# Kernel optimization log

Hardware: AMD Instinct MI355X
Metric: run time of the kernel (lower is better)

Reference implementation:

```python
import jax, jax.numpy as jnp
import numpy as np

D_MODEL = 512
NUM_HEADS = 8


def setup_inputs() -> dict:
    key = jax.random.key(0)
    ks = jax.random.split(key, 12)
    B, S, D = 2, 4096, D_MODEL
    scale = 1.0 / np.sqrt(D)
    inp = {
        "q": jax.random.normal(ks[0], (B, S, D), jnp.float32),
        "k": jax.random.normal(ks[1], (B, S, D), jnp.float32),
        "v": jax.random.normal(ks[2], (B, S, D), jnp.float32),
        "w_q": jax.random.normal(ks[3], (D, D), jnp.float32) * scale,
        "b_q": jax.random.normal(ks[4], (D,), jnp.float32) * scale,
        "w_k": jax.random.normal(ks[5], (D, D), jnp.float32) * scale,
        "b_k": jax.random.normal(ks[6], (D,), jnp.float32) * scale,
        "w_v": jax.random.normal(ks[7], (D, D), jnp.float32) * scale,
        "b_v": jax.random.normal(ks[8], (D,), jnp.float32) * scale,
        "w_o": jax.random.normal(ks[9], (D, D), jnp.float32) * scale,
        "b_o": jax.random.normal(ks[10], (D,), jnp.float32) * scale,
    }
    return inp


def _split_heads(x, h):
    b, s, d = x.shape
    return x.reshape(b, s, h, d // h).transpose(0, 2, 1, 3)  # [B,H,S,dk]


def reference(q, k, v, w_q, b_q, w_k, b_k, w_v, b_v, w_o, b_o):
    h = NUM_HEADS
    # Linear projections (torch Linear: x @ W.T + b)
    qh = _split_heads(q @ w_q.T + b_q, h)
    kh = _split_heads(k @ w_k.T + b_k, h)
    vh = _split_heads(v @ w_v.T + b_v, h)
    d_k = kh.shape[-1]
    scores = jnp.einsum("bhsd,bhtd->bhst", qh, kh) / jnp.sqrt(jnp.float32(d_k))
    attn = jax.nn.softmax(scores, axis=-1)  # [B,H,S,S] - materialized, as in source
    out = jnp.einsum("bhst,bhtd->bhsd", attn, vh)
    b, _, s, dk = out.shape
    out = out.transpose(0, 2, 1, 3).reshape(b, s, h * dk)
    return out @ w_o.T + b_o
```

## Files before the change

kernel.cpp:

```cpp
#include <hip/hip_runtime.h>
#include <hip/hip_bf16.h>

#define D_MODEL 512
#define NHEAD   8
#define DK      64
#define SEQ     4096
#define BATCH   2

typedef __bf16 bf16;
typedef __bf16 bf16x4 __attribute__((ext_vector_type(4)));
typedef __bf16 bf16x8 __attribute__((ext_vector_type(8)));
typedef float  f32x4  __attribute__((ext_vector_type(4)));

#define MFMA16(a, b, c) __builtin_amdgcn_mfma_f32_16x16x32_bf16((a), (b), (c), 0, 0, 0)

__global__ __launch_bounds__(256, 2) void proj_qkv(
    const float* __restrict__ q, const float* __restrict__ k, const float* __restrict__ v,
    const float* __restrict__ wq, const float* __restrict__ bq,
    const float* __restrict__ wk, const float* __restrict__ bk,
    const float* __restrict__ wv, const float* __restrict__ bv,
    bf16* __restrict__ Qh, bf16* __restrict__ Kh, bf16* __restrict__ Vt)
{
    const int p = blockIdx.z;
    const float* X    = (p == 0) ? q  : (p == 1) ? k  : v;
    const float* W    = (p == 0) ? wq : (p == 1) ? wk : wv;
    const float* bias = (p == 0) ? bq : (p == 1) ? bk : bv;

    __shared__ bf16 As[128][72];
    __shared__ bf16 Bs[128][72];

    const int m0   = blockIdx.x * 128;
    const int n0   = blockIdx.y * 128;
    const int tid  = threadIdx.x;
    const int lane = tid & 63;
    const int wave = tid >> 6;
    const int low4 = lane & 15;
    const int quad = lane >> 4;
    const int wm   = wave >> 1;
    const int wn   = wave & 1;

    int srow[8], sc4[8];
    for (int it = 0; it < 8; ++it) {
        int idx = tid + it * 256;
        srow[it] = idx >> 4;
        sc4[it]  = (idx & 15) * 4;
    }

    float4 gA[8], gB[8];
    for (int it = 0; it < 8; ++it) {
        gA[it] = *(const float4*)(X + (size_t)(m0 + srow[it]) * D_MODEL + sc4[it]);
        gB[it] = *(const float4*)(W + (size_t)(n0 + srow[it]) * D_MODEL + sc4[it]);
    }

    f32x4 acc[4][4];
    for (int i = 0; i < 4; ++i)
        for (int j = 0; j < 4; ++j)
            acc[i][j] = f32x4{0.f, 0.f, 0.f, 0.f};

    for (int k0 = 0; k0 < D_MODEL; k0 += 64) {
        __syncthreads();
        for (int it = 0; it < 8; ++it) {
            bf16x4 wa = {(bf16)gA[it].x, (bf16)gA[it].y, (bf16)gA[it].z, (bf16)gA[it].w};
            *(bf16x4*)&As[srow[it]][sc4[it]] = wa;
            bf16x4 wb = {(bf16)gB[it].x, (bf16)gB[it].y, (bf16)gB[it].z, (bf16)gB[it].w};
            *(bf16x4*)&Bs[srow[it]][sc4[it]] = wb;
        }
        __syncthreads();

        if (k0 + 64 < D_MODEL) {
            for (int it = 0; it < 8; ++it) {
                gA[it] = *(const float4*)(X + (size_t)(m0 + srow[it]) * D_MODEL + k0 + 64 + sc4[it]);
                gB[it] = *(const float4*)(W + (size_t)(n0 + srow[it]) * D_MODEL + k0 + 64 + sc4[it]);
            }
        }

        for (int ks = 0; ks < 2; ++ks) {
            bf16x8 a[4], b[4];
            for (int i = 0; i < 4; ++i)
                a[i] = *(const bf16x8*)&As[wm * 64 + i * 16 + low4][ks * 32 + quad * 8];
            for (int j = 0; j < 4; ++j)
                b[j] = *(const bf16x8*)&Bs[wn * 64 + j * 16 + low4][ks * 32 + quad * 8];
            for (int i = 0; i < 4; ++i)
                for (int j = 0; j < 4; ++j)
                    acc[i][j] = MFMA16(a[i], b[j], acc[i][j]);
        }
    }

    if (p < 2) {
        bf16* Out = (p == 0) ? Qh : Kh;
        const float sc = (p == 0) ? 0.125f : 1.0f;
        for (int j = 0; j < 4; ++j) {
            int col = n0 + wn * 64 + j * 16 + low4;
            float bcol = bias[col];
            for (int i = 0; i < 4; ++i)
                for (int r = 0; r < 4; ++r) {
                    int row = m0 + wm * 64 + i * 16 + quad * 4 + r;
                    Out[(size_t)row * D_MODEL + col] = (bf16)((acc[i][j][r] + bcol) * sc);
                }
        }
    } else {
        for (int j = 0; j < 4; ++j) {
            int col = n0 + wn * 64 + j * 16 + low4;
            float bcol = bias[col];
            int h = col >> 6, d = col & 63;
            for (int i = 0; i < 4; ++i)
                for (int r = 0; r < 4; ++r) {
                    int row = m0 + wm * 64 + i * 16 + quad * 4 + r;
                    int bb = row >> 12;
                    int s  = row & 4095;
                    Vt[(((size_t)(bb * NHEAD + h) * DK + d) << 12) + s] =
                        (bf16)(acc[i][j][r] + bcol);
                }
        }
    }
}

__global__ __launch_bounds__(256, 2) void attn(
    const bf16* __restrict__ Qh, const bf16* __restrict__ Kh,
    const bf16* __restrict__ Vt, bf16* __restrict__ O)
{
    __shared__ bf16 Ks[64][72];
    __shared__ bf16 Vs[64][72];
    __shared__ bf16 Ps[4][16][76];

    const int q0   = blockIdx.x * 128;
    const int bh   = blockIdx.y;
    const int b    = bh >> 3, h = bh & 7;
    const int tid  = threadIdx.x;
    const int lane = tid & 63;
    const int wave = tid >> 6;
    const int low4 = lane & 15;
    const int quad = lane >> 4;

    const bf16* Kbase = Kh + (size_t)b * SEQ * D_MODEL + h * DK;
    const bf16* Vbase = Vt + (size_t)bh * DK * SEQ;

    int srow[2], sg[2];
    for (int it = 0; it < 2; ++it) {
        int idx = tid + it * 256;
        srow[it] = idx >> 3;
        sg[it]   = idx & 7;
    }

    bf16x8 qf[2][2];
    for (int c = 0; c < 2; ++c) {
        const bf16* Qrow = Qh + (size_t)(b * SEQ + q0 + wave * 32 + c * 16 + low4) * D_MODEL + h * DK;
        qf[c][0] = *(const bf16x8*)(Qrow + quad * 8);
        qf[c][1] = *(const bf16x8*)(Qrow + 32 + quad * 8);
    }

    float l_c[2] = {0.f, 0.f};
    f32x4 acc_o[2][4];
    for (int c = 0; c < 2; ++c)
        for (int dt = 0; dt < 4; ++dt)
            acc_o[c][dt] = f32x4{0.f, 0.f, 0.f, 0.f};

    bf16x8 gk[2], gv[2];
    for (int it = 0; it < 2; ++it) {
        gk[it] = *(const bf16x8*)(Kbase + (size_t)srow[it] * D_MODEL + sg[it] * 8);
        gv[it] = *(const bf16x8*)(Vbase + (size_t)srow[it] * SEQ + sg[it] * 8);
    }

    const float L2E = 1.44269504f;

    for (int t0 = 0; t0 < SEQ; t0 += 64) {
        __syncthreads();
        for (int it = 0; it < 2; ++it) {
            *(bf16x8*)&Ks[srow[it]][sg[it] * 8] = gk[it];
            *(bf16x8*)&Vs[srow[it]][sg[it] * 8] = gv[it];
        }
        __syncthreads();

        bf16x8 kf[4][2], vf[4][2];
        for (int j = 0; j < 4; ++j)
            for (int ks = 0; ks < 2; ++ks) {
                kf[j][ks] = *(const bf16x8*)&Ks[j * 16 + low4][ks * 32 + quad * 8];
                vf[j][ks] = *(const bf16x8*)&Vs[j * 16 + low4][ks * 32 + quad * 8];
            }

        if (t0 + 64 < SEQ) {
            for (int it = 0; it < 2; ++it) {
                gk[it] = *(const bf16x8*)(Kbase + (size_t)(t0 + 64 + srow[it]) * D_MODEL + sg[it] * 8);
                gv[it] = *(const bf16x8*)(Vbase + (size_t)srow[it] * SEQ + t0 + 64 + sg[it] * 8);
            }
        }

        for (int c = 0; c < 2; ++c) {
            f32x4 sc[4];
            for (int j = 0; j < 4; ++j) sc[j] = f32x4{0.f, 0.f, 0.f, 0.f};
            for (int ks = 0; ks < 2; ++ks)
                for (int j = 0; j < 4; ++j)
                    sc[j] = MFMA16(kf[j][ks], qf[c][ks], sc[j]);

            for (int j = 0; j < 4; ++j) {
                float p0 = __builtin_amdgcn_exp2f(__builtin_fmaf(sc[j][0], L2E, -20.f));
                float p1 = __builtin_amdgcn_exp2f(__builtin_fmaf(sc[j][1], L2E, -20.f));
                float p2 = __builtin_amdgcn_exp2f(__builtin_fmaf(sc[j][2], L2E, -20.f));
                float p3 = __builtin_amdgcn_exp2f(__builtin_fmaf(sc[j][3], L2E, -20.f));
                l_c[c] += (p0 + p1) + (p2 + p3);
                bf16x4 pw = {(bf16)p0, (bf16)p1, (bf16)p2, (bf16)p3};
                *(bf16x4*)&Ps[wave][low4][j * 16 + quad * 4] = pw;
            }

            bf16x8 pf0 = *(const bf16x8*)&Ps[wave][low4][quad * 8];
            bf16x8 pf1 = *(const bf16x8*)&Ps[wave][low4][32 + quad * 8];
            for (int dt = 0; dt < 4; ++dt) {
                acc_o[c][dt] = MFMA16(pf0, vf[dt][0], acc_o[c][dt]);
                acc_o[c][dt] = MFMA16(pf1, vf[dt][1], acc_o[c][dt]);
            }
        }
    }

    for (int c = 0; c < 2; ++c) {
        float l = l_c[c];
        l += __shfl_xor(l, 16);
        l += __shfl_xor(l, 32);
        float inv = 1.0f / l;
        float invr[4];
        for (int r = 0; r < 4; ++r)
            invr[r] = __shfl(inv, quad * 4 + r);
        int rowb = b * SEQ + q0 + wave * 32 + c * 16;
        for (int dt = 0; dt < 4; ++dt)
            for (int r = 0; r < 4; ++r)
                O[(size_t)(rowb + quad * 4 + r) * D_MODEL + h * DK + dt * 16 + low4] =
                    (bf16)(acc_o[c][dt][r] * invr[r]);
    }
}

__global__ __launch_bounds__(256, 2) void proj_out(
    const bf16* __restrict__ Oin, const float* __restrict__ wo,
    const float* __restrict__ bo, float* __restrict__ out)
{
    __shared__ bf16 As[128][72];
    __shared__ bf16 Bs[128][72];

    const int m0   = blockIdx.x * 128;
    const int n0   = blockIdx.y * 128;
    const int tid  = threadIdx.x;
    const int lane = tid & 63;
    const int wave = tid >> 6;
    const int low4 = lane & 15;
    const int quad = lane >> 4;
    const int wm   = wave >> 1;
    const int wn   = wave & 1;

    int arow[4], ag[4];
    for (int it = 0; it < 4; ++it) {
        int idx = tid + it * 256;
        arow[it] = idx >> 3;
        ag[it]   = idx & 7;
    }
    int brow[8], bc4[8];
    for (int it = 0; it < 8; ++it) {
        int idx = tid + it * 256;
        brow[it] = idx >> 4;
        bc4[it]  = (idx & 15) * 4;
    }

    bf16x8 gA[4];
    float4 gB[8];
    for (int it = 0; it < 4; ++it)
        gA[it] = *(const bf16x8*)(Oin + (size_t)(m0 + arow[it]) * D_MODEL + ag[it] * 8);
    for (int it = 0; it < 8; ++it)
        gB[it] = *(const float4*)(wo + (size_t)(n0 + brow[it]) * D_MODEL + bc4[it]);

    f32x4 acc[4][4];
    for (int i = 0; i < 4; ++i)
        for (int j = 0; j < 4; ++j)
            acc[i][j] = f32x4{0.f, 0.f, 0.f, 0.f};

    for (int k0 = 0; k0 < D_MODEL; k0 += 64) {
        __syncthreads();
        for (int it = 0; it < 4; ++it)
            *(bf16x8*)&As[arow[it]][ag[it] * 8] = gA[it];
        for (int it = 0; it < 8; ++it) {
            bf16x4 wb = {(bf16)gB[it].x, (bf16)gB[it].y, (bf16)gB[it].z, (bf16)gB[it].w};
            *(bf16x4*)&Bs[brow[it]][bc4[it]] = wb;
        }
        __syncthreads();

        if (k0 + 64 < D_MODEL) {
            for (int it = 0; it < 4; ++it)
                gA[it] = *(const bf16x8*)(Oin + (size_t)(m0 + arow[it]) * D_MODEL + k0 + 64 + ag[it] * 8);
            for (int it = 0; it < 8; ++it)
                gB[it] = *(const float4*)(wo + (size_t)(n0 + brow[it]) * D_MODEL + k0 + 64 + bc4[it]);
        }

        for (int ks = 0; ks < 2; ++ks) {
            bf16x8 a[4], b[4];
            for (int i = 0; i < 4; ++i)
                a[i] = *(const bf16x8*)&As[wm * 64 + i * 16 + low4][ks * 32 + quad * 8];
            for (int j = 0; j < 4; ++j)
                b[j] = *(const bf16x8*)&Bs[wn * 64 + j * 16 + low4][ks * 32 + quad * 8];
            for (int i = 0; i < 4; ++i)
                for (int j = 0; j < 4; ++j)
                    acc[i][j] = MFMA16(a[i], b[j], acc[i][j]);
        }
    }

    for (int j = 0; j < 4; ++j) {
        int col = n0 + wn * 64 + j * 16 + low4;
        float bcol = bo[col];
        for (int i = 0; i < 4; ++i)
            for (int r = 0; r < 4; ++r) {
                int row = m0 + wm * 64 + i * 16 + quad * 4 + r;
                out[(size_t)row * D_MODEL + col] = acc[i][j][r] + bcol;
            }
    }
}

extern "C" void kernel_launch(void* const* d_in, const int* in_sizes, int n_in,
                              void* d_out, int out_size, void* d_ws, size_t ws_size,
                              hipStream_t stream)
{
    const float* q  = (const float*)d_in[0];
    const float* k  = (const float*)d_in[1];
    const float* v  = (const float*)d_in[2];
    const float* wq = (const float*)d_in[3];
    const float* bq = (const float*)d_in[4];
    const float* wk = (const float*)d_in[5];
    const float* bk = (const float*)d_in[6];
    const float* wv = (const float*)d_in[7];
    const float* bv = (const float*)d_in[8];
    const float* wo = (const float*)d_in[9];
    const float* bo = (const float*)d_in[10];

    const size_t NTOK = (size_t)BATCH * SEQ;
    bf16* Qh = (bf16*)d_ws;
    bf16* Kh = Qh + NTOK * D_MODEL;
    bf16* Vt = Kh + NTOK * D_MODEL;
    bf16* O  = Vt + (size_t)BATCH * NHEAD * DK * SEQ;

    dim3 g1(NTOK / 128, D_MODEL / 128, 3);
    proj_qkv<<<g1, 256, 0, stream>>>(q, k, v, wq, bq, wk, bk, wv, bv, Qh, Kh, Vt);

    dim3 g2(SEQ / 128, BATCH * NHEAD);
    attn<<<g2, 256, 0, stream>>>(Qh, Kh, Vt, O);

    dim3 g3(NTOK / 128, D_MODEL / 128);
    proj_out<<<g3, 256, 0, stream>>>(O, wo, bo, (float*)d_out);
}
```

Before: 243.7 us.

## Split attention over keys, stage V transpose in LDS, shrink output-proj tiles

```diff
diff --git a/kernel.cpp b/kernel.cpp
--- a/kernel.cpp
+++ b/kernel.cpp
@@ -6,6 +6,7 @@
 #define DK      64
 #define SEQ     4096
 #define BATCH   2
+#define NTOK    (BATCH * SEQ)
 
 typedef __bf16 bf16;
 typedef __bf16 bf16x4 __attribute__((ext_vector_type(4)));
@@ -14,7 +15,9 @@
 
 #define MFMA16(a, b, c) __builtin_amdgcn_mfma_f32_16x16x32_bf16((a), (b), (c), 0, 0, 0)
 
-__global__ __launch_bounds__(256, 2) void proj_qkv(
+#define QSCALE 0.18033688f
+
+__global__ __launch_bounds__(256, 3) void proj_qkv(
     const float* __restrict__ q, const float* __restrict__ k, const float* __restrict__ v,
     const float* __restrict__ wq, const float* __restrict__ bq,
     const float* __restrict__ wk, const float* __restrict__ bk,
@@ -26,8 +29,10 @@
     const float* W    = (p == 0) ? wq : (p == 1) ? wk : wv;
     const float* bias = (p == 0) ? bq : (p == 1) ? bk : bv;
 
-    __shared__ bf16 As[128][72];
-    __shared__ bf16 Bs[128][72];
+    __shared__ union __align__(16) {
+        struct { bf16 As[128][72]; bf16 Bs[128][72]; } g;
+        bf16 T[128][136];
+    } sm;
 
     const int m0   = blockIdx.x * 128;
     const int n0   = blockIdx.y * 128;
@@ -46,11 +51,9 @@
         sc4[it]  = (idx & 15) * 4;
     }
 
-    float4 gA[8], gB[8];
-    for (int it = 0; it < 8; ++it) {
+    float4 gA[8];
+    for (int it = 0; it < 8; ++it)
         gA[it] = *(const float4*)(X + (size_t)(m0 + srow[it]) * D_MODEL + sc4[it]);
-        gB[it] = *(const float4*)(W + (size_t)(n0 + srow[it]) * D_MODEL + sc4[it]);
-    }
 
     f32x4 acc[4][4];
     for (int i = 0; i < 4; ++i)
@@ -61,25 +64,23 @@
         __syncthreads();
         for (int it = 0; it < 8; ++it) {
             bf16x4 wa = {(bf16)gA[it].x, (bf16)gA[it].y, (bf16)gA[it].z, (bf16)gA[it].w};
-            *(bf16x4*)&As[srow[it]][sc4[it]] = wa;
-            bf16x4 wb = {(bf16)gB[it].x, (bf16)gB[it].y, (bf16)gB[it].z, (bf16)gB[it].w};
-            *(bf16x4*)&Bs[srow[it]][sc4[it]] = wb;
-        }
-        __syncthreads();
-
-        if (k0 + 64 < D_MODEL) {
-            for (int it = 0; it < 8; ++it) {
+            *(bf16x4*)&sm.g.As[srow[it]][sc4[it]] = wa;
+            float4 wv4 = *(const float4*)(W + (size_t)(n0 + srow[it]) * D_MODEL + k0 + sc4[it]);
+            bf16x4 wb = {(bf16)wv4.x, (bf16)wv4.y, (bf16)wv4.z, (bf16)wv4.w};
+            *(bf16x4*)&sm.g.Bs[srow[it]][sc4[it]] = wb;
+        }
+        __syncthreads();
+
+        if (k0 + 64 < D_MODEL)
+            for (int it = 0; it < 8; ++it)
                 gA[it] = *(const float4*)(X + (size_t)(m0 + srow[it]) * D_MODEL + k0 + 64 + sc4[it]);
-                gB[it] = *(const float4*)(W + (size_t)(n0 + srow[it]) * D_MODEL + k0 + 64 + sc4[it]);
-            }
-        }
 
         for (int ks = 0; ks < 2; ++ks) {
             bf16x8 a[4], b[4];
             for (int i = 0; i < 4; ++i)
-                a[i] = *(const bf16x8*)&As[wm * 64 + i * 16 + low4][ks * 32 + quad * 8];
+                a[i] = *(const bf16x8*)&sm.g.As[wm * 64 + i * 16 + low4][ks * 32 + quad * 8];
             for (int j = 0; j < 4; ++j)
-                b[j] = *(const bf16x8*)&Bs[wn * 64 + j * 16 + low4][ks * 32 + quad * 8];
+                b[j] = *(const bf16x8*)&sm.g.Bs[wn * 64 + j * 16 + low4][ks * 32 + quad * 8];
             for (int i = 0; i < 4; ++i)
                 for (int j = 0; j < 4; ++j)
                     acc[i][j] = MFMA16(a[i], b[j], acc[i][j]);
@@ -88,7 +89,7 @@
 
     if (p < 2) {
         bf16* Out = (p == 0) ? Qh : Kh;
-        const float sc = (p == 0) ? 0.125f : 1.0f;
+        const float sc = (p == 0) ? QSCALE : 1.0f;
         for (int j = 0; j < 4; ++j) {
             int col = n0 + wn * 64 + j * 16 + low4;
             float bcol = bias[col];
@@ -99,25 +100,33 @@
                 }
         }
     } else {
+        __syncthreads();
         for (int j = 0; j < 4; ++j) {
             int col = n0 + wn * 64 + j * 16 + low4;
             float bcol = bias[col];
-            int h = col >> 6, d = col & 63;
             for (int i = 0; i < 4; ++i)
-                for (int r = 0; r < 4; ++r) {
-                    int row = m0 + wm * 64 + i * 16 + quad * 4 + r;
-                    int bb = row >> 12;
-                    int s  = row & 4095;
-                    Vt[(((size_t)(bb * NHEAD + h) * DK + d) << 12) + s] =
+                for (int r = 0; r < 4; ++r)
+                    sm.T[wn * 64 + j * 16 + low4][wm * 64 + i * 16 + quad * 4 + r] =
                         (bf16)(acc[i][j][r] + bcol);
-                }
+        }
+        __syncthreads();
+        const int bb = m0 >> 12;
+        const int s0 = (m0 & 4095);
+        for (int it = 0; it < 8; ++it) {
+            int cc = it * 16 + (tid >> 4);
+            int ml = (tid & 15) * 8;
+            int col = n0 + cc;
+            int hh = col >> 6, dd = col & 63;
+            *(bf16x8*)&Vt[(((size_t)(bb * NHEAD + hh) * DK + dd) << 12) + s0 + ml] =
+                *(const bf16x8*)&sm.T[cc][ml];
         }
     }
 }
 
-__global__ __launch_bounds__(256, 2) void attn(
+__global__ __launch_bounds__(256, 4) void attn(
     const bf16* __restrict__ Qh, const bf16* __restrict__ Kh,
-    const bf16* __restrict__ Vt, bf16* __restrict__ O)
+    const bf16* __restrict__ Vt, bf16* __restrict__ Op,
+    float* __restrict__ lsum, int TK, int norm)
 {
     __shared__ bf16 Ks[64][72];
     __shared__ bf16 Vs[64][72];
@@ -126,12 +135,17 @@
     const int q0   = blockIdx.x * 128;
     const int bh   = blockIdx.y;
     const int b    = bh >> 3, h = bh & 7;
+    const int z    = blockIdx.z;
+    const int tbeg = z * TK, tend = tbeg + TK;
     const int tid  = threadIdx.x;
     const int lane = tid & 63;
     const int wave = tid >> 6;
     const int low4 = lane & 15;
     const int quad = lane >> 4;
 
+    bf16*  Oz = Op   + (size_t)z * NTOK * D_MODEL;
+    float* Lz = lsum + (size_t)z * NHEAD * BATCH * SEQ;
+
     const bf16* Kbase = Kh + (size_t)b * SEQ * D_MODEL + h * DK;
     const bf16* Vbase = Vt + (size_t)bh * DK * SEQ;
 
@@ -157,13 +171,11 @@
 
     bf16x8 gk[2], gv[2];
     for (int it = 0; it < 2; ++it) {
-        gk[it] = *(const bf16x8*)(Kbase + (size_t)srow[it] * D_MODEL + sg[it] * 8);
-        gv[it] = *(const bf16x8*)(Vbase + (size_t)srow[it] * SEQ + sg[it] * 8);
-    }
-
-    const float L2E = 1.44269504f;
-
-    for (int t0 = 0; t0 < SEQ; t0 += 64) {
+        gk[it] = *(const bf16x8*)(Kbase + (size_t)(tbeg + srow[it]) * D_MODEL + sg[it] * 8);
+        gv[it] = *(const bf16x8*)(Vbase + (size_t)srow[it] * SEQ + tbeg + sg[it] * 8);
+    }
+
+    for (int t0 = tbeg; t0 < tend; t0 += 64) {
         __syncthreads();
         for (int it = 0; it < 2; ++it) {
             *(bf16x8*)&Ks[srow[it]][sg[it] * 8] = gk[it];
@@ -178,7 +190,7 @@
                 vf[j][ks] = *(const bf16x8*)&Vs[j * 16 + low4][ks * 32 + quad * 8];
             }
 
-        if (t0 + 64 < SEQ) {
+        if (t0 + 64 < tend) {
             for (int it = 0; it < 2; ++it) {
                 gk[it] = *(const bf16x8*)(Kbase + (size_t)(t0 + 64 + srow[it]) * D_MODEL + sg[it] * 8);
                 gv[it] = *(const bf16x8*)(Vbase + (size_t)srow[it] * SEQ + t0 + 64 + sg[it] * 8);
@@ -193,10 +205,10 @@
                     sc[j] = MFMA16(kf[j][ks], qf[c][ks], sc[j]);
 
             for (int j = 0; j < 4; ++j) {
-                float p0 = __builtin_amdgcn_exp2f(__builtin_fmaf(sc[j][0], L2E, -20.f));
-                float p1 = __builtin_amdgcn_exp2f(__builtin_fmaf(sc[j][1], L2E, -20.f));
-                float p2 = __builtin_amdgcn_exp2f(__builtin_fmaf(sc[j][2], L2E, -20.f));
-                float p3 = __builtin_amdgcn_exp2f(__builtin_fmaf(sc[j][3], L2E, -20.f));
+                float p0 = __builtin_amdgcn_exp2f(sc[j][0]);
+                float p1 = __builtin_amdgcn_exp2f(sc[j][1]);
+                float p2 = __builtin_amdgcn_exp2f(sc[j][2]);
+                float p3 = __builtin_amdgcn_exp2f(sc[j][3]);
                 l_c[c] += (p0 + p1) + (p2 + p3);
                 bf16x4 pw = {(bf16)p0, (bf16)p1, (bf16)p2, (bf16)p3};
                 *(bf16x4*)&Ps[wave][low4][j * 16 + quad * 4] = pw;
@@ -215,27 +227,64 @@
         float l = l_c[c];
         l += __shfl_xor(l, 16);
         l += __shfl_xor(l, 32);
-        float inv = 1.0f / l;
-        float invr[4];
-        for (int r = 0; r < 4; ++r)
-            invr[r] = __shfl(inv, quad * 4 + r);
         int rowb = b * SEQ + q0 + wave * 32 + c * 16;
-        for (int dt = 0; dt < 4; ++dt)
+        if (norm) {
+            float inv = 1.0f / l;
+            float invr[4];
             for (int r = 0; r < 4; ++r)
-                O[(size_t)(rowb + quad * 4 + r) * D_MODEL + h * DK + dt * 16 + low4] =
-                    (bf16)(acc_o[c][dt][r] * invr[r]);
+                invr[r] = __shfl(inv, quad * 4 + r);
+            for (int dt = 0; dt < 4; ++dt)
+                for (int r = 0; r < 4; ++r)
+                    Oz[(size_t)(rowb + quad * 4 + r) * D_MODEL + h * DK + dt * 16 + low4] =
+                        (bf16)(acc_o[c][dt][r] * invr[r]);
+        } else {
+            if (quad == 0)
+                Lz[(size_t)bh * SEQ + q0 + wave * 32 + c * 16 + low4] = l;
+            for (int dt = 0; dt < 4; ++dt)
+                for (int r = 0; r < 4; ++r)
+                    Oz[(size_t)(rowb + quad * 4 + r) * D_MODEL + h * DK + dt * 16 + low4] =
+                        (bf16)acc_o[c][dt][r];
+        }
     }
 }
 
-__global__ __launch_bounds__(256, 2) void proj_out(
+__global__ __launch_bounds__(256) void combine(
+    bf16* __restrict__ Op, const float* __restrict__ lsum, int KS)
+{
+    size_t gi = (size_t)blockIdx.x * 256 + threadIdx.x;
+    int row  = (int)(gi >> 6);
+    int g    = (int)(gi & 63);
+    int head = g >> 3;
+    int bb   = row >> 12, s = row & 4095;
+    int bh   = bb * NHEAD + head;
+
+    float l = lsum[(size_t)bh * SEQ + s];
+    for (int z = 1; z < KS; ++z)
+        l += lsum[(size_t)z * NHEAD * BATCH * SEQ + (size_t)bh * SEQ + s];
+    float inv = 1.0f / l;
+
+    size_t off = (size_t)row * D_MODEL + g * 8;
+    bf16x8 o0 = *(const bf16x8*)(Op + off);
+    float acc[8];
+    for (int i = 0; i < 8; ++i) acc[i] = (float)o0[i];
+    for (int z = 1; z < KS; ++z) {
+        bf16x8 oz = *(const bf16x8*)(Op + (size_t)z * NTOK * D_MODEL + off);
+        for (int i = 0; i < 8; ++i) acc[i] += (float)oz[i];
+    }
+    bf16x8 w;
+    for (int i = 0; i < 8; ++i) w[i] = (bf16)(acc[i] * inv);
+    *(bf16x8*)(Op + off) = w;
+}
+
+__global__ __launch_bounds__(256, 4) void proj_out(
     const bf16* __restrict__ Oin, const float* __restrict__ wo,
     const float* __restrict__ bo, float* __restrict__ out)
 {
-    __shared__ bf16 As[128][72];
-    __shared__ bf16 Bs[128][72];
-
-    const int m0   = blockIdx.x * 128;
-    const int n0   = blockIdx.y * 128;
+    __shared__ bf16 As[64][72];
+    __shared__ bf16 Bs[64][72];
+
+    const int m0   = blockIdx.x * 64;
+    const int n0   = blockIdx.y * 64;
     const int tid  = threadIdx.x;
     const int lane = tid & 63;
     const int wave = tid >> 6;
@@ -244,66 +293,66 @@
     const int wm   = wave >> 1;
     const int wn   = wave & 1;
 
-    int arow[4], ag[4];
-    for (int it = 0; it < 4; ++it) {
+    int arow[2], ag[2];
+    for (int it = 0; it < 2; ++it) {
         int idx = tid + it * 256;
         arow[it] = idx >> 3;
         ag[it]   = idx & 7;
     }
-    int brow[8], bc4[8];
-    for (int it = 0; it < 8; ++it) {
+    int brow[4], bc4[4];
+    for (int it = 0; it < 4; ++it) {
         int idx = tid + it * 256;
         brow[it] = idx >> 4;
         bc4[it]  = (idx & 15) * 4;
     }
 
-    bf16x8 gA[4];
-    float4 gB[8];
+    bf16x8 gA[2];
+    float4 gB[4];
+    for (int it = 0; it < 2; ++it)
+        gA[it] = *(const bf16x8*)(Oin + (size_t)(m0 + arow[it]) * D_MODEL + ag[it] * 8);
     for (int it = 0; it < 4; ++it)
-        gA[it] = *(const bf16x8*)(Oin + (size_t)(m0 + arow[it]) * D_MODEL + ag[it] * 8);
-    for (int it = 0; it < 8; ++it)
         gB[it] = *(const float4*)(wo + (size_t)(n0 + brow[it]) * D_MODEL + bc4[it]);
 
-    f32x4 acc[4][4];
-    for (int i = 0; i < 4; ++i)
-        for (int j = 0; j < 4; ++j)
+    f32x4 acc[2][2];
+    for (int i = 0; i < 2; ++i)
+        for (int j = 0; j < 2; ++j)
             acc[i][j] = f32x4{0.f, 0.f, 0.f, 0.f};
 
     for (int k0 = 0; k0 < D_MODEL; k0 += 64) {
         __syncthreads();
-        for (int it = 0; it < 4; ++it)
+        for (int it = 0; it < 2; ++it)
             *(bf16x8*)&As[arow[it]][ag[it] * 8] = gA[it];
-        for (int it = 0; it < 8; ++it) {
+        for (int it = 0; it < 4; ++it) {
             bf16x4 wb = {(bf16)gB[it].x, (bf16)gB[it].y, (bf16)gB[it].z, (bf16)gB[it].w};
             *(bf16x4*)&Bs[brow[it]][bc4[it]] = wb;
         }
         __syncthreads();
 
         if (k0 + 64 < D_MODEL) {
+            for (int it = 0; it < 2; ++it)
+                gA[it] = *(const bf16x8*)(Oin + (size_t)(m0 + arow[it]) * D_MODEL + k0 + 64 + ag[it] * 8);
             for (int it = 0; it < 4; ++it)
-                gA[it] = *(const bf16x8*)(Oin + (size_t)(m0 + arow[it]) * D_MODEL + k0 + 64 + ag[it] * 8);
-            for (int it = 0; it < 8; ++it)
                 gB[it] = *(const float4*)(wo + (size_t)(n0 + brow[it]) * D_MODEL + k0 + 64 + bc4[it]);
         }
 
         for (int ks = 0; ks < 2; ++ks) {
-            bf16x8 a[4], b[4];
-            for (int i = 0; i < 4; ++i)
-                a[i] = *(const bf16x8*)&As[wm * 64 + i * 16 + low4][ks * 32 + quad * 8];
-            for (int j = 0; j < 4; ++j)
-                b[j] = *(const bf16x8*)&Bs[wn * 64 + j * 16 + low4][ks * 32 + quad * 8];
-            for (int i = 0; i < 4; ++i)
-                for (int j = 0; j < 4; ++j)
+            bf16x8 a[2], b[2];
+            for (int i = 0; i < 2; ++i)
+                a[i] = *(const bf16x8*)&As[wm * 32 + i * 16 + low4][ks * 32 + quad * 8];
+            for (int j = 0; j < 2; ++j)
+                b[j] = *(const bf16x8*)&Bs[wn * 32 + j * 16 + low4][ks * 32 + quad * 8];
+            for (int i = 0; i < 2; ++i)
+                for (int j = 0; j < 2; ++j)
                     acc[i][j] = MFMA16(a[i], b[j], acc[i][j]);
         }
     }
 
-    for (int j = 0; j < 4; ++j) {
-        int col = n0 + wn * 64 + j * 16 + low4;
+    for (int j = 0; j < 2; ++j) {
+        int col = n0 + wn * 32 + j * 16 + low4;
         float bcol = bo[col];
-        for (int i = 0; i < 4; ++i)
+        for (int i = 0; i < 2; ++i)
             for (int r = 0; r < 4; ++r) {
-                int row = m0 + wm * 64 + i * 16 + quad * 4 + r;
+                int row = m0 + wm * 32 + i * 16 + quad * 4 + r;
                 out[(size_t)row * D_MODEL + col] = acc[i][j][r] + bcol;
             }
     }
@@ -325,18 +374,28 @@
     const float* wo = (const float*)d_in[9];
     const float* bo = (const float*)d_in[10];
 
-    const size_t NTOK = (size_t)BATCH * SEQ;
+    const size_t NT = (size_t)NTOK * D_MODEL;
+    const size_t need2 = 5 * NT * sizeof(bf16)
+                       + (size_t)2 * NHEAD * BATCH * SEQ * sizeof(float);
+    const int KS = (ws_size >= need2) ? 2 : 1;
+
     bf16* Qh = (bf16*)d_ws;
-    bf16* Kh = Qh + NTOK * D_MODEL;
-    bf16* Vt = Kh + NTOK * D_MODEL;
-    bf16* O  = Vt + (size_t)BATCH * NHEAD * DK * SEQ;
+    bf16* Kh = Qh + NT;
+    bf16* Vt = Kh + NT;
+    bf16* Op = Vt + NT;
+    float* lsum = (float*)(Op + (size_t)KS * NT);
 
     dim3 g1(NTOK / 128, D_MODEL / 128, 3);
     proj_qkv<<<g1, 256, 0, stream>>>(q, k, v, wq, bq, wk, bk, wv, bv, Qh, Kh, Vt);
 
-    dim3 g2(SEQ / 128, BATCH * NHEAD);
-    attn<<<g2, 256, 0, stream>>>(Qh, Kh, Vt, O);
-
-    dim3 g3(NTOK / 128, D_MODEL / 128);
-    proj_out<<<g3, 256, 0, stream>>>(O, wo, bo, (float*)d_out);
+    dim3 g2(SEQ / 128, BATCH * NHEAD, KS);
+    attn<<<g2, 256, 0, stream>>>(Qh, Kh, Vt, Op, lsum, SEQ / KS, KS == 1 ? 1 : 0);
+
+    if (KS > 1) {
+        dim3 gc((NT / 8) / 256);
+        combine<<<gc, 256, 0, stream>>>(Op, lsum, KS);
+    }
+
+    dim3 g3(NTOK / 64, D_MODEL / 64);
+    proj_out<<<g3, 256, 0, stream>>>(Op, wo, bo, (float*)d_out);
 }
```

Measured after the change: 526.3 us. 116% more time.
